# Kernel optimization log

Hardware: AMD Instinct MI355X
Metric: run time of the kernel (lower is better)

The kernel has to match this reference:

```python
import jax, jax.numpy as jnp
import numpy as np

POOLING_COUNTS = [15, 8, 8]
N_CLIPS = 64


def build_mask_and_indices(pooling_counts, N):
    """Replicates the static index construction in __init__ (pure numpy)."""
    mask2d = np.zeros((N, N), dtype=bool)
    mask2d[np.arange(N), np.arange(N)] = True
    maskij = []
    pool_specs = []  # (kernel, stride) for each level
    for gi, c in enumerate(pooling_counts):
        if gi == 0:
            pool_specs.extend([(2, 1)] * c)
        else:
            pool_specs.extend([(3, 2)] + [(2, 1)] * (c - 1))
    stride, offset = 1, 0
    for c in pooling_counts:
        for _ in range(c):
            offset += stride
            i = np.arange(0, N - offset, stride)
            j = np.arange(offset, N, stride)
            mask2d[i, j] = True
            maskij.append((i, j))
        stride *= 2
    return mask2d, maskij, pool_specs


def maxpool1d(x, k, s):
    # x: [B, D, L]; MaxPool1d(kernel=k, stride=s), no padding
    L = x.shape[-1]
    out_len = (L - k) // s + 1
    idx = np.arange(out_len)[:, None] * s + np.arange(k)[None, :]  # [out_len, k]
    return x[..., idx].max(axis=-1)


def setup_inputs() -> dict:
    key = jax.random.key(0)
    x = jax.random.normal(key, (16, 512, N_CLIPS), dtype=jnp.float32)
    return {"x": x}


def reference(x):
    B, D, N = x.shape
    mask2d_np, maskij, pool_specs = build_mask_and_indices(POOLING_COUNTS, N)
    diag = np.arange(N)

    # diagonal scatter: map2d[:, :, n, n] = x[:, :, n]
    base = jnp.zeros((B, D, N, N), dtype=x.dtype).at[:, :, diag, diag].set(x)

    # boundary map: average of endpoint features at each (i, j) line
    boundary_map2d = base
    for i, j in maskij:
        boundary_map2d = boundary_map2d.at[:, :, i, j].set((x[:, :, i] + x[:, :, j]) * 0.5)

    # content map: pyramid of max-pools scattered onto the same lines
    content_map2d = base
    xp = x
    for (k, s), (i, j) in zip(pool_specs, maskij):
        xp = maxpool1d(xp, k, s)
        content_map2d = content_map2d.at[:, :, i, j].set(xp)

    mask2d = jnp.broadcast_to(jnp.asarray(mask2d_np)[None, None], (B, 1, N, N))
    return boundary_map2d, content_map2d, mask2d
```

## Files before the change

### kernel.cpp

```cpp
#include <hip/hip_runtime.h>


typedef float f32x4 __attribute__((ext_vector_type(4)));

__global__ __launch_bounds__(256) void sbc_kernel(const float* __restrict__ x,
                                                  float* __restrict__ out,
                                                  size_t mapsz) {
    const int lane = threadIdx.x & 63;
    const int wid  = blockIdx.x * 4 + (threadIdx.x >> 6);
    const int g    = lane >> 4;
    const int t    = lane & 15;
    const int j0   = t * 4;
    const int tile = wid * 4 + g;

    const float* xt = x + (size_t)tile * 64;

    float xall[64];
#pragma unroll
    for (int k = 0; k < 16; ++k) {
        f32x4 v = *(const f32x4*)(xt + 4 * k);
        xall[4 * k + 0] = v[0];
        xall[4 * k + 1] = v[1];
        xall[4 * k + 2] = v[2];
        xall[4 * k + 3] = v[3];
    }
    const f32x4 xj = *(const f32x4*)(xt + j0);

    unsigned long long mb[4];
#pragma unroll
    for (int c = 0; c < 4; ++c) {
        const int j  = j0 + c;
        const int sh = 63 - j;
        mb[c] = (1ULL << j)
              | (0x7FFF000000000000ULL >> sh)
              | ((0x0000555500000000ULL >> sh) & 0x5555555555555555ULL)
              | ((0x0000000011111111ULL >> sh) & 0x1111111111111111ULL);
    }

    const f32x4 xj05 = xj * 0.5f;
    float r[4];
#pragma unroll
    for (int c = 0; c < 4; ++c) r[c] = xj[c];

    float* __restrict__ bout = out + (size_t)tile * 4096 + j0;
    float* __restrict__ cout = bout + mapsz;

#pragma unroll
    for (int i = 63; i >= 0; --i) {
        const float xi   = xall[i];
        const float xi05 = xi * 0.5f;
        f32x4 bv, cv;
#pragma unroll
        for (int c = 0; c < 4; ++c) {
            const int j = j0 + c;
            const float xs = (j >= i) ? xi : -INFINITY;
            r[c] = fmaxf(r[c], xs);
            const bool on = (mb[c] >> i) & 1ULL;
            bv[c] = on ? (xi05 + xj05[c]) : 0.0f;
            cv[c] = on ? r[c] : 0.0f;
        }
        __builtin_nontemporal_store(bv, (f32x4*)(bout + i * 64));
        __builtin_nontemporal_store(cv, (f32x4*)(cout + i * 64));
    }

    if (g == 0 && (wid & 127) == 0) {
        float* __restrict__ mout = out + 2 * mapsz + (size_t)(wid >> 7) * 4096 + j0;
#pragma unroll
        for (int i = 0; i < 64; ++i) {
            f32x4 mv;
#pragma unroll
            for (int c = 0; c < 4; ++c)
                mv[c] = ((mb[c] >> i) & 1ULL) ? 1.0f : 0.0f;
            __builtin_nontemporal_store(mv, (f32x4*)(mout + i * 64));
        }
    }
}

extern "C" void kernel_launch(void* const* d_in, const int* in_sizes, int n_in,
                              void* d_out, int out_size, void* d_ws, size_t ws_size,
                              hipStream_t stream) {
    const float* x = (const float*)d_in[0];
    float* out = (float*)d_out;
    const int N  = 64;
    const int BD = in_sizes[0] / N;
    const size_t mapsz = (size_t)BD * N * N;
    const int nwaves = BD / 4;
    sbc_kernel<<<dim3(nwaves / 4), dim3(256), 0, stream>>>(x, out, mapsz);
}
```

Baseline: 266.7 us.

## Assign one wave per tile and share x rows via cross-lane shuffles

Each wave now handles a single 64x64 tile instead of four, with its four 16-lane groups taking interleaved rows (i = 4s+g). Each lane loads one x element and fetches row values with __shfl instead of holding all 64 values in registers, and the running max is rebuilt from 4-element prefix maxima with a per-column start step. The grid is four times larger and register pressure drops, which should raise occupancy. Stores change from nontemporal to ordinary and now cover four consecutive rows per instruction. This trades extra shuffle and select work for better parallelism and store coalescing.

```diff
diff --git a/kernel.cpp b/kernel.cpp
--- a/kernel.cpp
+++ b/kernel.cpp
@@ -9,69 +9,80 @@
     const int lane = threadIdx.x & 63;
     const int wid  = blockIdx.x * 4 + (threadIdx.x >> 6);
     const int g    = lane >> 4;
-    const int t    = lane & 15;
-    const int j0   = t * 4;
-    const int tile = wid * 4 + g;
+    const int j0   = (lane & 15) * 4;
+    const int tile = wid;
 
     const float* xt = x + (size_t)tile * 64;
-
-    float xall[64];
-#pragma unroll
-    for (int k = 0; k < 16; ++k) {
-        f32x4 v = *(const f32x4*)(xt + 4 * k);
-        xall[4 * k + 0] = v[0];
-        xall[4 * k + 1] = v[1];
-        xall[4 * k + 2] = v[2];
-        xall[4 * k + 3] = v[3];
-    }
+    const float xv = xt[lane];
     const f32x4 xj = *(const f32x4*)(xt + j0);
 
-    unsigned long long mb[4];
+    unsigned on16[4];
+    int sE[4], tE[4];
+    f32x4 hxj;
 #pragma unroll
     for (int c = 0; c < 4; ++c) {
         const int j  = j0 + c;
         const int sh = 63 - j;
-        mb[c] = (1ULL << j)
-              | (0x7FFF000000000000ULL >> sh)
-              | ((0x0000555500000000ULL >> sh) & 0x5555555555555555ULL)
-              | ((0x0000000011111111ULL >> sh) & 0x1111111111111111ULL);
+        const unsigned long long mb =
+              (1ULL << j)
+            | (0x7FFF000000000000ULL >> sh)
+            | ((0x0000555500000000ULL >> sh) & 0x5555555555555555ULL)
+            | ((0x0000000011111111ULL >> sh) & 0x1111111111111111ULL);
+        unsigned long long v = (mb >> g) & 0x1111111111111111ULL;
+        v |= v >> 3;  v &= 0x0303030303030303ULL;
+        v |= v >> 6;  v &= 0x000F000F000F000FULL;
+        v |= v >> 12; v &= 0x000000FF000000FFULL;
+        v |= v >> 24;
+        on16[c] = (unsigned)v & 0xFFFFu;
+        const int d = j - g;
+        sE[c] = d >> 2;
+        tE[c] = d & 3;
+        hxj[c] = 0.5f * xj[c];
     }
 
-    const f32x4 xj05 = xj * 0.5f;
     float r[4];
 #pragma unroll
     for (int c = 0; c < 4; ++c) r[c] = xj[c];
 
-    float* __restrict__ bout = out + (size_t)tile * 4096 + j0;
-    float* __restrict__ cout = bout + mapsz;
+    float* __restrict__ b0 = out + (size_t)tile * 4096 + g * 64 + j0;
+    float* __restrict__ c0 = b0 + mapsz;
 
 #pragma unroll
-    for (int i = 63; i >= 0; --i) {
-        const float xi   = xall[i];
-        const float xi05 = xi * 0.5f;
+    for (int s = 15; s >= 0; --s) {
+        const int i = 4 * s + g;
+        const float y0 = __shfl(xv, i, 64);
+        const float y1 = __shfl(xv, i + 1, 64);
+        const float y2 = __shfl(xv, i + 2, 64);
+        const float y3 = __shfl(xv, i + 3, 64);
+        const float P1 = fmaxf(y0, y1);
+        const float P2 = fmaxf(P1, y2);
+        const float P3 = fmaxf(P2, y3);
+        const float xi05 = 0.5f * y0;
         f32x4 bv, cv;
 #pragma unroll
         for (int c = 0; c < 4; ++c) {
-            const int j = j0 + c;
-            const float xs = (j >= i) ? xi : -INFINITY;
-            r[c] = fmaxf(r[c], xs);
-            const bool on = (mb[c] >> i) & 1ULL;
-            bv[c] = on ? (xi05 + xj05[c]) : 0.0f;
+            const float pick = tE[c] >= 3 ? P3
+                             : (tE[c] == 2 ? P2 : (tE[c] == 1 ? P1 : y0));
+            const float rn = fmaxf(r[c], P3);
+            r[c] = (s == sE[c]) ? pick : rn;
+            const bool on = (on16[c] >> s) & 1u;
+            bv[c] = on ? (xi05 + hxj[c]) : 0.0f;
             cv[c] = on ? r[c] : 0.0f;
         }
-        __builtin_nontemporal_store(bv, (f32x4*)(bout + i * 64));
-        __builtin_nontemporal_store(cv, (f32x4*)(cout + i * 64));
+        *(f32x4*)(b0 + s * 256) = bv;
+        *(f32x4*)(c0 + s * 256) = cv;
     }
 
-    if (g == 0 && (wid & 127) == 0) {
-        float* __restrict__ mout = out + 2 * mapsz + (size_t)(wid >> 7) * 4096 + j0;
+    if ((wid & 511) == 0) {
+        float* __restrict__ m0 = out + 2 * mapsz + (size_t)(wid >> 9) * 4096
+                               + g * 64 + j0;
 #pragma unroll
-        for (int i = 0; i < 64; ++i) {
+        for (int s = 0; s < 16; ++s) {
             f32x4 mv;
 #pragma unroll
             for (int c = 0; c < 4; ++c)
-                mv[c] = ((mb[c] >> i) & 1ULL) ? 1.0f : 0.0f;
-            __builtin_nontemporal_store(mv, (f32x4*)(mout + i * 64));
+                mv[c] = ((on16[c] >> s) & 1u) ? 1.0f : 0.0f;
+            *(f32x4*)(m0 + s * 256) = mv;
         }
     }
 }
@@ -84,6 +95,5 @@
     const int N  = 64;
     const int BD = in_sizes[0] / N;
     const size_t mapsz = (size_t)BD * N * N;
-    const int nwaves = BD / 4;
-    sbc_kernel<<<dim3(nwaves / 4), dim3(256), 0, stream>>>(x, out, mapsz);
+    sbc_kernel<<<dim3(BD / 4), dim3(256), 0, stream>>>(x, out, mapsz);
 }
```

Measured after the change: 256.2 us. 4.0% less time.
